# Optimization experiments

Hardware: AMD Instinct MI355X
Metric: run time of the kernel (lower is better)

## Reference

```python
import jax, jax.numpy as jnp
import numpy as np

B, L, E, H = 4, 1024, 1024, 16
DH = E // H
EPS = 1e-5


def _linear(x, W, b):
    # torch nn.Linear: x @ W.T + b, W: (out, in)
    return jnp.einsum('ble,oe->blo', x, W) + b


def _layernorm(x, g, b):
    m = jnp.mean(x, axis=-1, keepdims=True)
    v = jnp.var(x, axis=-1, keepdims=True)
    return (x - m) * jax.lax.rsqrt(v + EPS) * g + b


def setup_inputs() -> dict:
    key = jax.random.key(0)
    ks = jax.random.split(key, 16)
    s = 1.0 / np.sqrt(E)
    inp = {
        'x': jax.random.normal(ks[0], (B, L, E), dtype=jnp.float32),
        'mask': jax.random.randint(ks[1], (B, L), 0, 2, dtype=jnp.int32),
        'Wq': jax.random.uniform(ks[2], (E, E), jnp.float32, -s, s),
        'bq': jax.random.uniform(ks[3], (E,), jnp.float32, -s, s),
        'Wk': jax.random.uniform(ks[4], (E, E), jnp.float32, -s, s),
        'bk': jax.random.uniform(ks[5], (E,), jnp.float32, -s, s),
        'Wv': jax.random.uniform(ks[6], (E, E), jnp.float32, -s, s),
        'bv': jax.random.uniform(ks[7], (E,), jnp.float32, -s, s),
        'Wo': jax.random.uniform(ks[8], (E, E), jnp.float32, -s, s),
        'bo': jax.random.uniform(ks[9], (E,), jnp.float32, -s, s),
        'g1': jnp.ones((E,), jnp.float32),
        'b1': jnp.zeros((E,), jnp.float32),
        'Wf': jax.random.uniform(ks[10], (E, E), jnp.float32, -s, s),
        'bf': jax.random.uniform(ks[11], (E,), jnp.float32, -s, s),
        'g2': jnp.ones((E,), jnp.float32),
        'b2': jnp.zeros((E,), jnp.float32),
        'alpha': jnp.float32(0.5),
    }
    return inp


def reference(x, mask, Wq, bq, Wk, bk, Wv, bv, Wo, bo, g1, b1, Wf, bf, g2, b2, alpha):
    q = _linear(x, Wq, bq)
    k = _linear(x, Wk, bk)
    v = _linear(x, Wv, bv)
    # Faithful to source: reshape(B, H, L, -1) with NO transpose (non-standard head split)
    q = q.reshape(B, H, L, DH)
    k = k.reshape(B, H, L, DH)
    v = v.reshape(B, H, L, DH)
    scores = jnp.einsum('bhqd,bhkd->bhqk', q, k) / np.sqrt(DH).astype(np.float32)
    # mask (B,L) -> (B,1,1,L), fill -1e10 where mask == 0
    m = mask[:, None, None, :]
    scores = jnp.where(m == 0, jnp.float32(-1e10), scores)
    attn = jax.nn.softmax(scores, axis=-1)
    att = jnp.einsum('bhqk,bhkd->bhqd', attn, v)  # (B,H,L,DH)
    att = att.transpose(0, 2, 1, 3).reshape(B, L, E)
    att = _linear(att, Wo, bo)
    # dropout is identity in eval mode
    skip1 = _layernorm(x + att, g1, b1)
    fcc = jax.nn.gelu(_linear(skip1, Wf, bf), approximate=False)
    skip2 = _layernorm(skip1 + fcc, g2, b2)
    return x * alpha + skip2 * (1.0 - alpha)
```

## Files before the change

kernel.cpp:

```cpp
#include <hip/hip_runtime.h>
#include <hip/hip_bf16.h>
#include <string.h>

typedef __attribute__((ext_vector_type(8))) short short8;
typedef __attribute__((ext_vector_type(4))) float f32x4;
typedef __attribute__((ext_vector_type(4))) unsigned short u16x4;

#define MFMA_BF16(a, b, c) __builtin_amdgcn_mfma_f32_16x16x32_bf16((a), (b), (c), 0, 0, 0)

__device__ __forceinline__ unsigned short f2bf(float f) {
  unsigned int u = __builtin_bit_cast(unsigned int, f);
  u += 0x7fffu + ((u >> 16) & 1u);
  return (unsigned short)(u >> 16);
}

__device__ __forceinline__ float bf2f(unsigned short s) {
  unsigned int u = ((unsigned int)s) << 16;
  return __builtin_bit_cast(float, u);
}

__device__ __forceinline__ unsigned pk_bf16(float a, float b) {
  __hip_bfloat162 h = __float22bfloat162_rn(float2{a, b});
  unsigned r;
  memcpy(&r, &h, 4);
  return r;
}

__device__ __forceinline__ void gload_lds16(const void* g, void* lds) {
  __builtin_amdgcn_global_load_lds(
      (const __attribute__((address_space(1))) unsigned int*)g,
      (__attribute__((address_space(3))) unsigned int*)lds, 16, 0, 0);
}

__global__ __launch_bounds__(256) void cast_all(const float* __restrict__ x,
                                                const float* __restrict__ Wq,
                                                const float* __restrict__ Wk,
                                                const float* __restrict__ Wv,
                                                const float* __restrict__ Wo,
                                                const float* __restrict__ Wf,
                                                unsigned short* __restrict__ xb,
                                                unsigned short* __restrict__ Wqkv,
                                                unsigned short* __restrict__ Wob,
                                                unsigned short* __restrict__ Wfb,
                                                const int* __restrict__ mask,
                                                const float* __restrict__ bq,
                                                const float* __restrict__ bk,
                                                const float* __restrict__ bv,
                                                float* __restrict__ ma,
                                                float* __restrict__ bcat) {
  int i = blockIdx.x * 256 + threadIdx.x;
  if (i < 2359296) {
    const float* src;
    unsigned short* dst;
    int j;
    if (i < 1048576)      { src = x;  dst = xb;             j = i; }
    else if (i < 1310720) { src = Wq; dst = Wqkv;           j = i - 1048576; }
    else if (i < 1572864) { src = Wk; dst = Wqkv + 1048576; j = i - 1310720; }
    else if (i < 1835008) { src = Wv; dst = Wqkv + 2097152; j = i - 1572864; }
    else if (i < 2097152) { src = Wo; dst = Wob;            j = i - 1835008; }
    else                  { src = Wf; dst = Wfb;            j = i - 2097152; }
    float4 v = ((const float4*)src)[j];
    u16x4 r = { f2bf(v.x), f2bf(v.y), f2bf(v.z), f2bf(v.w) };
    ((u16x4*)dst)[j] = r;
  } else {
    int j = i - 2359296;
    if (j < 4096) ma[j] = (mask[j] == 0) ? -1.4426950408889634e10f : 0.0f;
    int k = j - 4096;
    if (k >= 0 && k < 3072) {
      float v = (k < 1024) ? bq[k] : (k < 2048 ? bk[k - 1024] : bv[k - 2048]);
      bcat[k] = v;
    }
  }
}

template <int EPI>
__global__ __launch_bounds__(256) void gemm_lds64(const unsigned short* __restrict__ A,
                                                  const unsigned short* __restrict__ W,
                                                  const float* __restrict__ bias,
                                                  void* __restrict__ Cout,
                                                  int M, int N, int K) {
  __shared__ unsigned short At[128 * 64];
  __shared__ unsigned short Bt[64 * 64];

  const int tid = threadIdx.x;
  const int w = tid >> 6, l = tid & 63;
  const int lr = l & 15, lq = l >> 4;
  const int row0 = blockIdx.x * 128;
  const int col0 = blockIdx.y * 64;

  const int sr8 = l >> 3;
  const int sc8 = ((l & 7) ^ (l >> 3)) * 8;

  f32x4 acc[2][4] = {};

  for (int kt = 0; kt < K; kt += 64) {
#pragma unroll
    for (int j = 0; j < 4; j++) {
      const int r = (w * 4 + j) * 8 + sr8;
      gload_lds16(A + (size_t)(row0 + r) * K + kt + sc8, &At[(w * 4 + j) * 512]);
    }
#pragma unroll
    for (int j = 0; j < 2; j++) {
      const int r = (w * 2 + j) * 8 + sr8;
      gload_lds16(W + (size_t)(col0 + r) * K + kt + sc8, &Bt[(w * 2 + j) * 512]);
    }
    __syncthreads();

    short8 af[2][2], bfr[2][4];
#pragma unroll
    for (int ks = 0; ks < 2; ks++) {
      const int slot = ((ks * 4 + lq) ^ (lr & 7)) * 8;
#pragma unroll
      for (int m = 0; m < 2; m++)
        af[ks][m] = *(const short8*)&At[(w * 32 + m * 16 + lr) * 64 + slot];
#pragma unroll
      for (int n = 0; n < 4; n++)
        bfr[ks][n] = *(const short8*)&Bt[(n * 16 + lr) * 64 + slot];
    }
#pragma unroll
    for (int ks = 0; ks < 2; ks++)
#pragma unroll
      for (int m = 0; m < 2; m++)
#pragma unroll
        for (int n = 0; n < 4; n++)
          acc[m][n] = MFMA_BF16(af[ks][m], bfr[ks][n], acc[m][n]);
    __syncthreads();
  }

#pragma unroll
  for (int n = 0; n < 4; n++) {
    const int col = col0 + n * 16 + lr;
    const float bv = bias[col];
#pragma unroll
    for (int m = 0; m < 2; m++) {
      const int row = row0 + w * 32 + m * 16 + lq * 4;
#pragma unroll
      for (int r = 0; r < 4; r++) {
        float v = acc[m][n][r] + bv;
        if (EPI == 0) {
          ((unsigned short*)Cout)[(size_t)(row + r) * N + col] = f2bf(v);
        } else {
          float g = 0.5f * v * (1.0f + erff(v * 0.70710678118654752f));
          ((unsigned short*)Cout)[(size_t)(row + r) * N + col] = f2bf(g);
        }
      }
    }
  }
}

__global__ __launch_bounds__(256) void vtrans_kernel(const unsigned short* __restrict__ qkv,
                                                     unsigned short* __restrict__ VT) {
  const int bh = blockIdx.x;
  const int kt = blockIdx.y;
  const int t = threadIdx.x;
  const int d = t & 63, kg = t >> 6;
  const unsigned short* basev =
      qkv + ((size_t)(bh >> 4) * 1024 + (bh & 15) * 64) * 3072 + 2048;
  const unsigned short* src = basev + (size_t)(kt * 4 + kg) * 3072 + d;
  unsigned short vals[16];
#pragma unroll
  for (int j = 0; j < 16; j++) vals[j] = src[j * 64];
  short8 v0, v1;
#pragma unroll
  for (int j = 0; j < 8; j++) { v0[j] = (short)vals[j]; v1[j] = (short)vals[8 + j]; }
  size_t dst = ((size_t)bh * 64 + d) * 1024 + kt * 64 + kg * 16;
  *(short8*)&VT[dst] = v0;
  *(short8*)&VT[dst + 8] = v1;
}

__global__ __launch_bounds__(256) void attn14_kernel(const unsigned short* __restrict__ qkv,
                                                     const unsigned short* __restrict__ VT,
                                                     const float* __restrict__ maskadd,
                                                     unsigned short* __restrict__ att) {
  __shared__ unsigned short Kt[3][2048];
  __shared__ unsigned short Vt[3][2048];
  __shared__ float ma_lds[1024];
  __shared__ unsigned short Pl[4][640];

  const int bh = blockIdx.x, b = bh >> 4, h = bh & 15;
  const int qb = blockIdx.y;
  const int tid = threadIdx.x, w = tid >> 6, l = tid & 63;
  const int lr = l & 15, lq = l >> 4;

  const unsigned short* baseq = qkv + ((size_t)b * 1024 + h * 64) * 3072;
  const unsigned short* basek = baseq + 1024;
  const unsigned short* vtb = VT + (size_t)bh * 64 * 1024;

  const int skey = (tid >> 2) & 31;
  const int skd = (tid >> 7) * 32 + (((tid & 3) ^ ((skey >> 1) & 3)) * 8);
  const int svd = tid >> 2;
  const int svc = ((tid & 3) ^ ((svd >> 1) & 3)) * 8;

  short8 qf[2];
  const int q0 = qb * 64 + w * 16;
  {
    const int p = q0 + lr;
    const unsigned short* qa = baseq + (p >> 4) * 3072 + (p & 15) * 64;
    qf[0] = *(const short8*)(qa + lq * 8);
    qf[1] = *(const short8*)(qa + 32 + lq * 8);
  }
  ((float4*)ma_lds)[tid] = ((const float4*)(maskadd + b * 1024))[tid];

#pragma unroll
  for (int t0 = 0; t0 < 2; t0++) {
    const int pk = t0 * 32 + skey;
    gload_lds16(basek + (pk >> 4) * 3072 + (pk & 15) * 64 + skd, (char*)&Kt[t0][0] + w * 1024);
    gload_lds16(vtb + (size_t)svd * 1024 + t0 * 32 + svc, (char*)&Vt[t0][0] + w * 1024);
  }
  asm volatile("s_waitcnt lgkmcnt(0) vmcnt(2)" ::: "memory");
  __builtin_amdgcn_s_barrier();
  __builtin_amdgcn_sched_barrier(0);

  float ll = 0.f;
  f32x4 o[4] = {};
  unsigned short* pw = &Pl[w][0];
  constexpr float SC = 0.18033688011112042f;
  const int cx = (lq ^ ((lr >> 1) & 3)) * 8;

#pragma unroll 1
  for (int kt = 0; kt < 32; kt++) {
    const int cur = kt % 3;
    if (kt < 30) {
      const int st = (kt + 2) % 3;
      const int pk = (kt + 2) * 32 + skey;
      gload_lds16(basek + (pk >> 4) * 3072 + (pk & 15) * 64 + skd,
                  (char*)&Kt[st][0] + w * 1024);
      gload_lds16(vtb + (size_t)svd * 1024 + (kt + 2) * 32 + svc,
                  (char*)&Vt[st][0] + w * 1024);
    }

    const unsigned short* KtL = &Kt[cur][0];
    const unsigned short* VtL = &Vt[cur][0];
    short8 vf[4];
#pragma unroll
    for (int n = 0; n < 4; n++)
      vf[n] = *(const short8*)&VtL[(n * 16 + lr) * 32 + cx];

    const float4 mk0 = *(const float4*)&ma_lds[kt * 32 + lq * 4];
    const float4 mk1 = *(const float4*)&ma_lds[kt * 32 + 16 + lq * 4];

    short8 kf00 = *(const short8*)&KtL[lr * 32 + cx];
    short8 kf01 = *(const short8*)&KtL[1024 + lr * 32 + cx];
    short8 kf10 = *(const short8*)&KtL[(16 + lr) * 32 + cx];
    short8 kf11 = *(const short8*)&KtL[1024 + (16 + lr) * 32 + cx];
    f32x4 s0 = {0.f, 0.f, 0.f, 0.f}, s1 = {0.f, 0.f, 0.f, 0.f};
    __builtin_amdgcn_s_setprio(1);
    s0 = MFMA_BF16(kf00, qf[0], s0);
    s0 = MFMA_BF16(kf01, qf[1], s0);
    s1 = MFMA_BF16(kf10, qf[0], s1);
    s1 = MFMA_BF16(kf11, qf[1], s1);
    __builtin_amdgcn_s_setprio(0);

    float p[8], rs = 0.f;
#pragma unroll
    for (int r = 0; r < 4; r++) {
      p[r]     = __builtin_amdgcn_exp2f(s0[r] * SC + ((const float*)&mk0)[r]);
      p[4 + r] = __builtin_amdgcn_exp2f(s1[r] * SC + ((const float*)&mk1)[r]);
    }
#pragma unroll
    for (int i = 0; i < 8; i++) rs += p[i];
    ll += rs;

    uint2 wa, wb;
    wa.x = pk_bf16(p[0], p[1]);
    wa.y = pk_bf16(p[2], p[3]);
    wb.x = pk_bf16(p[4], p[5]);
    wb.y = pk_bf16(p[6], p[7]);
    *(uint2*)&pw[lr * 40 + lq * 4] = wa;
    *(uint2*)&pw[lr * 40 + 16 + lq * 4] = wb;

    asm volatile("s_waitcnt lgkmcnt(0)" ::: "memory");
    const short8 pa = *(const short8*)&pw[lr * 40 + lq * 8];
    __builtin_amdgcn_s_setprio(1);
#pragma unroll
    for (int n = 0; n < 4; n++)
      o[n] = MFMA_BF16(pa, vf[n], o[n]);
    __builtin_amdgcn_s_setprio(0);

    if (kt < 30) {
      asm volatile("s_waitcnt vmcnt(2)" ::: "memory");
      __builtin_amdgcn_s_barrier();
      __builtin_amdgcn_sched_barrier(0);
    } else if (kt == 30) {
      asm volatile("s_waitcnt vmcnt(0)" ::: "memory");
      __builtin_amdgcn_s_barrier();
      __builtin_amdgcn_sched_barrier(0);
    }
  }

  float lf = ll;
  lf += __shfl_xor(lf, 16);
  lf += __shfl_xor(lf, 32);
  float inv[4];
#pragma unroll
  for (int r = 0; r < 4; r++) inv[r] = 1.0f / __shfl(lf, lq * 4 + r);
#pragma unroll
  for (int r = 0; r < 4; r++) {
    const int q = q0 + lq * 4 + r;
    const size_t obase = ((size_t)b * 1024 + q) * 1024 + h * 64;
#pragma unroll
    for (int n = 0; n < 4; n++)
      att[obase + n * 16 + lr] = f2bf(o[n][r] * inv[r]);
  }
}

__global__ __launch_bounds__(256) void ln1_kernel(const float* __restrict__ x,
                                                  const unsigned short* __restrict__ attp,
                                                  const float* __restrict__ g,
                                                  const float* __restrict__ bt,
                                                  unsigned short* __restrict__ sb) {
  const int row = blockIdx.x, tid = threadIdx.x;
  float4 xv = ((const float4*)(x + row * 1024))[tid];
  u16x4 ab = ((const u16x4*)(attp + row * 1024))[tid];
  float4 v = {xv.x + bf2f(ab[0]), xv.y + bf2f(ab[1]), xv.z + bf2f(ab[2]), xv.w + bf2f(ab[3])};
  float s = v.x + v.y + v.z + v.w;
  float sq = v.x * v.x + v.y * v.y + v.z * v.z + v.w * v.w;
#pragma unroll
  for (int off = 1; off < 64; off <<= 1) { s += __shfl_xor(s, off); sq += __shfl_xor(sq, off); }
  __shared__ float ws[8];
  int wv = tid >> 6, l = tid & 63;
  if (l == 0) { ws[wv] = s; ws[4 + wv] = sq; }
  __syncthreads();
  s = ws[0] + ws[1] + ws[2] + ws[3];
  sq = ws[4] + ws[5] + ws[6] + ws[7];
  float mean = s * (1.0f / 1024.0f);
  float var = sq * (1.0f / 1024.0f) - mean * mean;
  float rs = rsqrtf(var + 1e-5f);
  float4 gv = ((const float4*)g)[tid];
  float4 bv = ((const float4*)bt)[tid];
  u16x4 yb = { f2bf((v.x - mean) * rs * gv.x + bv.x),
               f2bf((v.y - mean) * rs * gv.y + bv.y),
               f2bf((v.z - mean) * rs * gv.z + bv.z),
               f2bf((v.w - mean) * rs * gv.w + bv.w) };
  ((u16x4*)(sb + row * 1024))[tid] = yb;
}

__global__ __launch_bounds__(256) void ln2_kernel(const unsigned short* __restrict__ skip,
                                                  const unsigned short* __restrict__ fcc,
                                                  const float* __restrict__ g,
                                                  const float* __restrict__ bt,
                                                  const float* __restrict__ x,
                                                  const float* __restrict__ alphap,
                                                  float* __restrict__ out) {
  const int row = blockIdx.x, tid = threadIdx.x;
  u16x4 sb = ((const u16x4*)(skip + row * 1024))[tid];
  u16x4 fb = ((const u16x4*)(fcc + row * 1024))[tid];
  float4 v = {bf2f(sb[0]) + bf2f(fb[0]), bf2f(sb[1]) + bf2f(fb[1]),
              bf2f(sb[2]) + bf2f(fb[2]), bf2f(sb[3]) + bf2f(fb[3])};
  float s = v.x + v.y + v.z + v.w;
  float sq = v.x * v.x + v.y * v.y + v.z * v.z + v.w * v.w;
#pragma unroll
  for (int off = 1; off < 64; off <<= 1) { s += __shfl_xor(s, off); sq += __shfl_xor(sq, off); }
  __shared__ float ws[8];
  int wv = tid >> 6, l = tid & 63;
  if (l == 0) { ws[wv] = s; ws[4 + wv] = sq; }
  __syncthreads();
  s = ws[0] + ws[1] + ws[2] + ws[3];
  sq = ws[4] + ws[5] + ws[6] + ws[7];
  float mean = s * (1.0f / 1024.0f);
  float var = sq * (1.0f / 1024.0f) - mean * mean;
  float rs = rsqrtf(var + 1e-5f);
  float4 gv = ((const float4*)g)[tid];
  float4 bv = ((const float4*)bt)[tid];
  float alpha = alphap[0];
  float beta = 1.0f - alpha;
  float4 xv = ((const float4*)(x + row * 1024))[tid];
  float4 y;
  y.x = xv.x * alpha + ((v.x - mean) * rs * gv.x + bv.x) * beta;
  y.y = xv.y * alpha + ((v.y - mean) * rs * gv.y + bv.y) * beta;
  y.z = xv.z * alpha + ((v.z - mean) * rs * gv.z + bv.z) * beta;
  y.w = xv.w * alpha + ((v.w - mean) * rs * gv.w + bv.w) * beta;
  ((float4*)(out + row * 1024))[tid] = y;
}

extern "C" void kernel_launch(void* const* d_in, const int* in_sizes, int n_in,
                              void* d_out, int out_size, void* d_ws, size_t ws_size,
                              hipStream_t stream) {
  const float* x  = (const float*)d_in[0];
  const int* mask = (const int*)d_in[1];
  const float* Wq = (const float*)d_in[2];
  const float* bq = (const float*)d_in[3];
  const float* Wk = (const float*)d_in[4];
  const float* bk = (const float*)d_in[5];
  const float* Wv = (const float*)d_in[6];
  const float* bv = (const float*)d_in[7];
  const float* Wo = (const float*)d_in[8];
  const float* bo = (const float*)d_in[9];
  const float* g1 = (const float*)d_in[10];
  const float* b1 = (const float*)d_in[11];
  const float* Wf = (const float*)d_in[12];
  const float* bf = (const float*)d_in[13];
  const float* g2 = (const float*)d_in[14];
  const float* b2 = (const float*)d_in[15];
  const float* alpha = (const float*)d_in[16];
  float* out = (float*)d_out;

  char* ws = (char*)d_ws;
  size_t off = 0;
  unsigned short* xb   = (unsigned short*)(ws + off); off += 8388608;
  unsigned short* Wqkv = (unsigned short*)(ws + off); off += 6291456;
  unsigned short* Wob  = (unsigned short*)(ws + off); off += 2097152;
  unsigned short* Wfb  = (unsigned short*)(ws + off); off += 2097152;
  float* bcat          = (float*)(ws + off);          off += 12288;
  float* maf           = (float*)(ws + off);          off += 16384;
  unsigned short* qkvb = (unsigned short*)(ws + off); off += 25165824;
  unsigned short* attb = (unsigned short*)(ws + off); off += 8388608;
  float* tmp           = (float*)(ws + off);          off += 16777216;
  unsigned short* s1b  = (unsigned short*)(ws + off); off += 8388608;

  unsigned short* VT  = (unsigned short*)tmp;
  unsigned short* obf = (unsigned short*)tmp;
  unsigned short* fbf = (unsigned short*)tmp + 4194304;

  cast_all<<<9244, 256, 0, stream>>>(x, Wq, Wk, Wv, Wo, Wf, xb, Wqkv, Wob, Wfb,
                                     mask, bq, bk, bv, maf, bcat);

  gemm_lds64<0><<<dim3(32, 48), 256, 0, stream>>>(xb, Wqkv, bcat, qkvb, 4096, 3072, 1024);

  vtrans_kernel<<<dim3(64, 16), 256, 0, stream>>>(qkvb, VT);

  attn14_kernel<<<dim3(64, 16), 256, 0, stream>>>(qkvb, VT, maf, attb);

  gemm_lds64<0><<<dim3(32, 16), 256, 0, stream>>>(attb, Wob, bo, obf, 4096, 1024, 1024);

  ln1_kernel<<<4096, 256, 0, stream>>>(x, obf, g1, b1, s1b);

  gemm_lds64<3><<<dim3(32, 16), 256, 0, stream>>>(s1b, Wfb, bf, fbf, 4096, 1024, 1024);

  ln2_kernel<<<4096, 256, 0, stream>>>(s1b, fbf, g2, b2, x, alpha, out);
}
```

Baseline: 144.1 us.

## Double-buffer LDS tiles in GEMM to overlap global loads with MFMA

The bf16 GEMM kernel now keeps two LDS stages for the A and W tiles and prefetches tile t+2 while computing tile t. It uses explicit vmcnt waits and raw barriers in place of two __syncthreads per iteration. It also raises wave priority around the MFMA block. The goal is to hide global-to-LDS load latency behind matrix math, at the cost of doubled LDS use (48KB) and possibly lower occupancy.

```diff
diff --git a/kernel.cpp b/kernel.cpp
--- a/kernel.cpp
+++ b/kernel.cpp
@@ -79,8 +79,8 @@
                                                   const float* __restrict__ bias,
                                                   void* __restrict__ Cout,
                                                   int M, int N, int K) {
-  __shared__ unsigned short At[128 * 64];
-  __shared__ unsigned short Bt[64 * 64];
+  __shared__ unsigned short At[2][128 * 64];
+  __shared__ unsigned short Bt[2][64 * 64];
 
   const int tid = threadIdx.x;
   const int w = tid >> 6, l = tid & 63;
@@ -91,20 +91,34 @@
   const int sr8 = l >> 3;
   const int sc8 = ((l & 7) ^ (l >> 3)) * 8;
 
+  const int NT = K >> 6;
+
+#define GSTAGE(s, t)                                                              \
+  {                                                                               \
+    const int kt_ = (t) * 64;                                                     \
+    _Pragma("unroll")                                                             \
+    for (int j = 0; j < 4; j++) {                                                 \
+      const int r_ = (w * 4 + j) * 8 + sr8;                                       \
+      gload_lds16(A + (size_t)(row0 + r_) * K + kt_ + sc8, &At[s][(w * 4 + j) * 512]); \
+    }                                                                             \
+    _Pragma("unroll")                                                             \
+    for (int j = 0; j < 2; j++) {                                                 \
+      const int r_ = (w * 2 + j) * 8 + sr8;                                       \
+      gload_lds16(W + (size_t)(col0 + r_) * K + kt_ + sc8, &Bt[s][(w * 2 + j) * 512]); \
+    }                                                                             \
+  }
+
+  GSTAGE(0, 0);
+  GSTAGE(1, 1);
+  asm volatile("s_waitcnt vmcnt(6)" ::: "memory");
+  __builtin_amdgcn_s_barrier();
+  __builtin_amdgcn_sched_barrier(0);
+
   f32x4 acc[2][4] = {};
 
-  for (int kt = 0; kt < K; kt += 64) {
-#pragma unroll
-    for (int j = 0; j < 4; j++) {
-      const int r = (w * 4 + j) * 8 + sr8;
-      gload_lds16(A + (size_t)(row0 + r) * K + kt + sc8, &At[(w * 4 + j) * 512]);
-    }
-#pragma unroll
-    for (int j = 0; j < 2; j++) {
-      const int r = (w * 2 + j) * 8 + sr8;
-      gload_lds16(W + (size_t)(col0 + r) * K + kt + sc8, &Bt[(w * 2 + j) * 512]);
-    }
-    __syncthreads();
+#pragma unroll 1
+  for (int t = 0; t < NT; t++) {
+    const int cur = t & 1;
 
     short8 af[2][2], bfr[2][4];
 #pragma unroll
@@ -112,11 +126,18 @@
       const int slot = ((ks * 4 + lq) ^ (lr & 7)) * 8;
 #pragma unroll
       for (int m = 0; m < 2; m++)
-        af[ks][m] = *(const short8*)&At[(w * 32 + m * 16 + lr) * 64 + slot];
+        af[ks][m] = *(const short8*)&At[cur][(w * 32 + m * 16 + lr) * 64 + slot];
 #pragma unroll
       for (int n = 0; n < 4; n++)
-        bfr[ks][n] = *(const short8*)&Bt[(n * 16 + lr) * 64 + slot];
-    }
+        bfr[ks][n] = *(const short8*)&Bt[cur][(n * 16 + lr) * 64 + slot];
+    }
+    asm volatile("s_waitcnt lgkmcnt(0)" ::: "memory");
+    __builtin_amdgcn_s_barrier();
+    __builtin_amdgcn_sched_barrier(0);
+
+    if (t + 2 < NT) GSTAGE(cur, t + 2);
+
+    __builtin_amdgcn_s_setprio(1);
 #pragma unroll
     for (int ks = 0; ks < 2; ks++)
 #pragma unroll
@@ -124,8 +145,19 @@
 #pragma unroll
         for (int n = 0; n < 4; n++)
           acc[m][n] = MFMA_BF16(af[ks][m], bfr[ks][n], acc[m][n]);
-    __syncthreads();
-  }
+    __builtin_amdgcn_s_setprio(0);
+
+    if (t + 2 < NT) {
+      asm volatile("s_waitcnt vmcnt(6)" ::: "memory");
+      __builtin_amdgcn_s_barrier();
+      __builtin_amdgcn_sched_barrier(0);
+    } else if (t + 2 == NT) {
+      asm volatile("s_waitcnt vmcnt(0)" ::: "memory");
+      __builtin_amdgcn_s_barrier();
+      __builtin_amdgcn_sched_barrier(0);
+    }
+  }
+#undef GSTAGE
 
 #pragma unroll
   for (int n = 0; n < 4; n++) {
```

Result: faster. 136.3 us, median of 3 (-5.4%).
